# Performance work log

Hardware: AMD Instinct MI355X
Metric: run time of the kernel (lower is better)

## Reference

```python
import jax, jax.numpy as jnp
import numpy as np

B, S, TK, H, E, V, OOV = 16, 8, 400, 256, 128, 50000, 50
H2 = 2 * H


def setup_inputs() -> dict:
    key = jax.random.key(0)
    ks = jax.random.split(key, 24)
    std = 0.02
    d = {}
    d["y_t_1"] = jax.random.randint(ks[0], (B,), 0, V)
    d["h0"] = jax.random.normal(ks[1], (B, H), jnp.float32)
    d["c0"] = jax.random.normal(ks[2], (B, H), jnp.float32)
    d["encoder_output"] = jax.random.normal(ks[3], (B, S, TK, H2), jnp.float32)
    d["section_output"] = jax.random.normal(ks[4], (B, S, H2), jnp.float32)
    d["enc_padding_mask"] = jnp.ones((B, S, TK), jnp.float32)
    d["c_t_1"] = jax.random.normal(ks[5], (B, H2), jnp.float32)
    d["extra_zeros"] = jnp.zeros((B, OOV), jnp.float32)
    d["enc_batch_extend_vocab"] = jax.random.randint(ks[6], (B, S * TK), 0, V + OOV)
    d["coverage"] = jnp.zeros((B, S, TK), jnp.float32)
    d["gamma"] = jnp.ones((B, S, TK), jnp.float32)
    # learned parameters
    d["embedding"] = std * jax.random.normal(ks[7], (V, E), jnp.float32)
    d["W_xc"] = std * jax.random.normal(ks[8], (H2 + E, E), jnp.float32)
    d["b_xc"] = jnp.zeros((E,), jnp.float32)
    d["W_ih"] = std * jax.random.normal(ks[9], (E, 4 * H), jnp.float32)
    d["b_ih"] = jnp.zeros((4 * H,), jnp.float32)
    d["W_hh"] = std * jax.random.normal(ks[10], (H, 4 * H), jnp.float32)
    # pytorch init sets forget-gate bias (2nd quarter) to 1
    d["b_hh"] = jnp.zeros((4 * H,), jnp.float32).at[H:2 * H].set(1.0)
    d["Wh_sec"] = std * jax.random.normal(ks[11], (H2, H2), jnp.float32)
    d["Wd_sec"] = std * jax.random.normal(ks[12], (H2, H2), jnp.float32)
    d["bd_sec"] = jnp.zeros((H2,), jnp.float32)
    d["v_sec"] = std * jax.random.normal(ks[13], (H2, 1), jnp.float32)
    d["Wh_w"] = std * jax.random.normal(ks[14], (H2, H2), jnp.float32)
    d["Wc_w"] = std * jax.random.normal(ks[15], (H2,), jnp.float32)
    d["Wd_w"] = std * jax.random.normal(ks[16], (H2, H2), jnp.float32)
    d["bd_w"] = jnp.zeros((H2,), jnp.float32)
    d["v_w"] = std * jax.random.normal(ks[17], (H2, 1), jnp.float32)
    d["W_pgen"] = std * jax.random.normal(ks[18], (4 * H + E, 1), jnp.float32)
    d["b_pgen"] = jnp.zeros((1,), jnp.float32)
    d["W_out1"] = std * jax.random.normal(ks[19], (3 * H, H), jnp.float32)
    d["b_out1"] = jnp.zeros((H,), jnp.float32)
    d["W_out2"] = std * jax.random.normal(ks[20], (H, V), jnp.float32)
    d["b_out2"] = jnp.zeros((V,), jnp.float32)
    return d


def reference(y_t_1, h0, c0, encoder_output, section_output, enc_padding_mask,
              c_t_1, extra_zeros, enc_batch_extend_vocab, coverage, gamma,
              embedding, W_xc, b_xc, W_ih, b_ih, W_hh, b_hh,
              Wh_sec, Wd_sec, bd_sec, v_sec,
              Wh_w, Wc_w, Wd_w, bd_w, v_w,
              W_pgen, b_pgen, W_out1, b_out1, W_out2, b_out2):
    # embedding + input context projection
    emb = embedding[y_t_1]                                      # [B,E]
    x = jnp.concatenate([c_t_1, emb], axis=1) @ W_xc + b_xc     # [B,E]
    # single-step LSTM (pytorch gate order i,f,g,o)
    gates = x @ W_ih + b_ih + h0 @ W_hh + b_hh                  # [B,4H]
    i, f, g, o = jnp.split(gates, 4, axis=1)
    c = jax.nn.sigmoid(f) * c0 + jax.nn.sigmoid(i) * jnp.tanh(g)
    h = jax.nn.sigmoid(o) * jnp.tanh(c)
    s_t_hat = jnp.concatenate([h, c], axis=1)                   # [B,2H]
    # section attention -> beta [B,S]
    e_sec = jnp.tanh(section_output @ Wh_sec + (s_t_hat @ Wd_sec + bd_sec)[:, None, :])
    sc_sec = jnp.squeeze(e_sec @ v_sec, -1)                     # [B,S]
    beta = jax.nn.softmax(sc_sec, axis=1)
    beta = beta / beta.sum(axis=1, keepdims=True)
    # word attention with coverage feature
    att = encoder_output @ Wh_w + (s_t_hat @ Wd_w + bd_w)[:, None, None, :]
    att = att + coverage[..., None] * Wc_w                      # [B,S,TK,2H]
    sc_w = jnp.squeeze(jnp.tanh(att) @ v_w, -1)                 # [B,S,TK]
    ws = (beta[:, :, None] * sc_w).reshape(B, S * TK)
    mask = enc_padding_mask.reshape(B, S * TK)
    ad = jax.nn.softmax(ws, axis=1) * mask
    attn = ad / ad.sum(axis=1, keepdims=True)                   # [B,S*TK]
    c_t = jnp.einsum('bt,btn->bn', attn, encoder_output.reshape(B, S * TK, H2))
    cov = coverage + attn.reshape(B, S, TK)
    # pointer-gen gate
    p_gen = jax.nn.sigmoid(jnp.concatenate([c_t, s_t_hat, x], axis=1) @ W_pgen + b_pgen)  # [B,1]
    # output vocab distribution
    out = jnp.concatenate([h, c_t], axis=1) @ W_out1 + b_out1
    vocab_dist = jax.nn.softmax(out @ W_out2 + b_out2, axis=1)  # [B,V]
    vd = jnp.concatenate([p_gen * vocab_dist, extra_zeros], axis=1)  # [B,V+OOV]
    ad_ = (1.0 - p_gen) * attn
    rows = jnp.arange(B)[:, None]
    final_dist = vd.at[rows, enc_batch_extend_vocab].add(ad_)
    return (final_dist, h, c, c_t, attn, p_gen, cov)
```

## Files before the change

kernel.cpp:

```cpp
#include <hip/hip_runtime.h>
#include <math.h>

#define BB   16
#define SS   8
#define TKK  400
#define HH   256
#define EE   128
#define VV   50000
#define OOVV 50
#define HH2  512
#define STK  (SS*TKK)
#define VOO  (VV+OOVV)

#define OFF_X     0
#define OFF_ST    2048
#define OFF_SD    10240
#define OFF_WD    18432
#define OFF_SCSEC 26752
#define OFF_SCW   26880
#define OFF_CT    78080
#define OFF_OUT1  86272
#define OFF_PGEN  90368
#define OFF_PSUM  93520
#define OFF_BT    113040

#define O_FD   0
#define O_H    800800
#define O_C    804896
#define O_CT   808992
#define O_ATTN 817184
#define O_PGEN 868384
#define O_COV  868400

#define NLB 391
#define GEMM_NB 800

typedef __attribute__((ext_vector_type(8))) short bf16x8;
typedef __attribute__((ext_vector_type(4))) float f32x4;

__device__ __forceinline__ float sigm(float x){ return 1.0f/(1.0f+expf(-x)); }

__device__ __forceinline__ unsigned short f2b(float f){
  unsigned int u = __float_as_uint(f);
  unsigned int r = (u + 0x7fffu + ((u >> 16) & 1u)) >> 16;
  return (unsigned short)r;
}

__device__ __forceinline__ float tanhfast(float x){
  float cx = fminf(9.0f, fmaxf(-9.0f, x));
  float t = __expf(2.0f*cx);
  return (t - 1.0f) * __builtin_amdgcn_rcpf(t + 1.0f);
}

__device__ __forceinline__ float wave_sum(float v){
  #pragma unroll
  for(int o=32;o>0;o>>=1) v += __shfl_xor(v,o);
  return v;
}
__device__ __forceinline__ float wave_max(float v){
  #pragma unroll
  for(int o=32;o>0;o>>=1) v = fmaxf(v,__shfl_xor(v,o));
  return v;
}

__device__ __forceinline__ void glds16(const void* g, void* l){
  __builtin_amdgcn_global_load_lds((const __attribute__((address_space(1))) void*)g,
                                   (__attribute__((address_space(3))) void*)l, 16, 0, 0);
}

__device__ __forceinline__ bf16x8 cvt8(float4 a, float4 b){
  union{ bf16x8 v; unsigned short u[8]; } t;
  t.u[0]=f2b(a.x); t.u[1]=f2b(a.y); t.u[2]=f2b(a.z); t.u[3]=f2b(a.w);
  t.u[4]=f2b(b.x); t.u[5]=f2b(b.y); t.u[6]=f2b(b.z); t.u[7]=f2b(b.w);
  return t.v;
}

__global__ void k_pre(const float* __restrict__ Whw, unsigned short* __restrict__ Btg,
                      const int* __restrict__ y, const float* __restrict__ ct1,
                      const float* __restrict__ emb, const float* __restrict__ Wxc,
                      const float* __restrict__ bxc, const float* __restrict__ bdsec,
                      const float* __restrict__ bdw, float* __restrict__ ws){
  __shared__ float sm[10440];
  int bi = blockIdx.x, tid = threadIdx.x;
  if(bi < 64){
    int n0 = (bi & 7)*64, k0 = (bi >> 3)*64;
    int tx = tid & 63, ty = tid >> 6;
    #pragma unroll
    for(int it=0; it<16; it++){
      int kk = it*4 + ty;
      sm[kk*65 + tx] = Whw[(size_t)(k0+kk)*HH2 + n0 + tx];
    }
    __syncthreads();
    #pragma unroll
    for(int it=0; it<2; it++){
      int kgl = it*4 + ty;
      int kgG = (k0 >> 3) + kgl;
      int rnd = kgG >> 2, kg = kgG & 3;
      int col = n0 + tx;
      union{ bf16x8 v; unsigned short u[8]; } t;
      #pragma unroll
      for(int j=0;j<8;j++) t.u[j] = f2b(sm[(kgl*8+j)*65 + tx]);
      *(bf16x8*)&Btg[(size_t)rnd*16384 + (size_t)(col*4 + (kg ^ ((col>>1)&3)))*8] = t.v;
    }
  } else if(bi < 80){
    float* cat = sm;
    float* red = sm + 10240;
    for(int f=tid; f<BB*640; f+=256){
      int b = f/640, r = f - b*640;
      cat[f] = (r < HH2) ? ct1[b*HH2 + r] : emb[(size_t)y[b]*EE + (r-HH2)];
    }
    __syncthreads();
    int c = (bi-64)*8 + (tid & 7);
    int b = (tid >> 3) & 15;
    int kh = tid >> 7;
    float acc = 0.0f;
    const float* a = &cat[b*640];
    for(int k=kh*320; k<kh*320+320; k++) acc += a[k]*Wxc[k*EE + c];
    if(kh==1) red[b*8 + (tid&7)] = acc;
    __syncthreads();
    if(kh==0) ws[OFF_X + b*EE + c] = acc + red[b*8 + (tid&7)] + bxc[c];
  } else {
    for(int f=tid; f<BB*HH2; f+=256){
      int c = f & (HH2-1);
      ws[OFF_CT + f] = 0.0f;
      ws[OFF_SD + f] = bdsec[c];
      ws[OFF_WD + f] = bdw[c];
    }
  }
}

__global__ void k_lstm(const float* __restrict__ h0, const float* __restrict__ c0,
                       const float* __restrict__ Wih, const float* __restrict__ bih,
                       const float* __restrict__ Whh, const float* __restrict__ bhh,
                       float* __restrict__ ws, float* __restrict__ out){
  __shared__ float xh[4*384];
  __shared__ float red[3*64*4];
  int tid = threadIdx.x;
  int jc = (blockIdx.x & 15)*16, bc = (blockIdx.x >> 4)*4;
  for(int f=tid; f<4*384; f+=256){
    int bl = f/384, r = f - bl*384;
    xh[f] = (r < EE) ? ws[OFF_X + (bc+bl)*EE + r] : h0[(bc+bl)*HH + (r-EE)];
  }
  __syncthreads();
  int jl = tid & 15, bl = (tid >> 4) & 3, kq = tid >> 6;
  int j = jc + jl, b = bc + bl;
  float a0=0.f, a1=0.f, a2=0.f, a3=0.f;
  const float* a = &xh[bl*384];
  for(int k=kq*96; k<kq*96+96; k++){
    float v = a[k];
    const float* w = (k < EE) ? &Wih[k*4*HH + j] : &Whh[(k-EE)*4*HH + j];
    a0 += v*w[0]; a1 += v*w[HH]; a2 += v*w[2*HH]; a3 += v*w[3*HH];
  }
  if(kq){
    float* r = &red[((kq-1)*64 + bl*16 + jl)*4];
    r[0]=a0; r[1]=a1; r[2]=a2; r[3]=a3;
  }
  __syncthreads();
  if(kq==0){
    #pragma unroll
    for(int p=0;p<3;p++){
      const float* r = &red[(p*64 + bl*16 + jl)*4];
      a0+=r[0]; a1+=r[1]; a2+=r[2]; a3+=r[3];
    }
    a0 += bih[j] + bhh[j];
    a1 += bih[j+HH] + bhh[j+HH];
    a2 += bih[j+2*HH] + bhh[j+2*HH];
    a3 += bih[j+3*HH] + bhh[j+3*HH];
    float c = sigm(a1)*c0[b*HH+j] + sigm(a0)*tanhf(a2);
    float h = sigm(a3)*tanhf(c);
    out[O_H + b*HH + j] = h;
    out[O_C + b*HH + j] = c;
    ws[OFF_ST + b*HH2 + j]      = h;
    ws[OFF_ST + b*HH2 + HH + j] = c;
  }
}

__global__ void k_proj(const float* __restrict__ Wdsec, const float* __restrict__ Wdw,
                       float* __restrict__ ws){
  __shared__ float st[BB*32];
  int tid = threadIdx.x;
  int mi = blockIdx.x >> 5;
  int cb = (blockIdx.x >> 4) & 1;
  int kq = blockIdx.x & 15;
  int k0 = kq*32;
  for(int f=tid; f<BB*32; f+=256){
    int b = f >> 5, kk = f & 31;
    st[f] = ws[OFF_ST + b*HH2 + k0 + kk];
  }
  __syncthreads();
  int c = cb*256 + tid;
  const float* Wm = (mi ? Wdw : Wdsec) + (size_t)k0*HH2 + c;
  float acc[BB];
  #pragma unroll
  for(int b=0;b<BB;b++) acc[b] = 0.0f;
  #pragma unroll 4
  for(int kk=0;kk<32;kk++){
    float wv = Wm[(size_t)kk*HH2];
    #pragma unroll
    for(int b=0;b<BB;b++) acc[b] += st[b*32 + kk]*wv;
  }
  int dst = mi ? OFF_WD : OFF_SD;
  #pragma unroll
  for(int b=0;b<BB;b++) atomicAdd(&ws[dst + b*HH2 + c], acc[b]);
}

__global__ __launch_bounds__(512, 4) void k_gemm6(
        const float* __restrict__ A, const unsigned short* __restrict__ Btg,
        const float* __restrict__ Wcw, const float* __restrict__ vw,
        const float* __restrict__ cover,
        const float* __restrict__ sec, const float* __restrict__ Whsec,
        const float* __restrict__ vsec, float* __restrict__ ws){
  __shared__ __align__(16) unsigned short smem[32768];
  int tid = threadIdx.x;
  if(blockIdx.x >= GEMM_NB){
    float* row = (float*)smem;
    float* red = row + HH2;
    int bi = blockIdx.x - GEMM_NB;
    int b = bi >> 3;
    if(tid < HH2) row[tid] = sec[(size_t)bi*HH2 + tid];
    __syncthreads();
    int col = tid;
    float acc = 0.0f;
    #pragma unroll 8
    for(int k=0;k<HH2;k++) acc += row[k]*Whsec[k*HH2 + col];
    float val = tanhf(acc + ws[OFF_SD + b*HH2 + col]) * vsec[col];
    val = wave_sum(val);
    if((tid&63)==0) red[tid>>6] = val;
    __syncthreads();
    if(tid==0){
      float s = 0.0f;
      #pragma unroll
      for(int i=0;i<8;i++) s += red[i];
      ws[OFF_SCSEC + bi] = s;
    }
    return;
  }
  int w = tid >> 6, lane = tid & 63, m = lane & 15, q = lane >> 4;
  int mk = (m >> 1) & 3, sw = q ^ mk;
  int rg = w >> 2, cg = w & 3;
  int row0 = blockIdx.x * 64;
  int b = blockIdx.x / 50;

  const float* a0p = &A[(size_t)(row0 + rg*32 + m)*HH2 + q*8];
  const float* a1p = a0p + (size_t)16*HH2;

  f32x4 acc0[8], acc1[8];
  #pragma unroll
  for(int j=0;j<8;j++){ acc0[j] = (f32x4){0.f,0.f,0.f,0.f}; acc1[j] = (f32x4){0.f,0.f,0.f,0.f}; }

  float4 pa[2][4];
  bf16x8 af0, af1;

  #define GLDSB(rr, buf) {                                                     \
    const unsigned short* bsrc_ = Btg + (size_t)(rr)*16384;                    \
    unsigned short* ldst_ = &smem[(buf)*16384];                                \
    _Pragma("unroll")                                                          \
    for(int i_=0;i_<4;i_++)                                                    \
      glds16(bsrc_ + i_*4096 + tid*8, ldst_ + i_*4096 + tid*8);                \
  }
  #define LOADA(rr, s) {                                                       \
    pa[s][0] = *(const float4*)(a0p + (rr)*32);                                \
    pa[s][1] = *(const float4*)(a0p + (rr)*32 + 4);                            \
    pa[s][2] = *(const float4*)(a1p + (rr)*32);                                \
    pa[s][3] = *(const float4*)(a1p + (rr)*32 + 4);                            \
  }

  GLDSB(0, 0);
  LOADA(0, 0);
  LOADA(1, 1);
  GLDSB(1, 1);
  asm volatile("s_waitcnt vmcnt(8)" ::: "memory");
  __builtin_amdgcn_sched_barrier(0);
  af0 = cvt8(pa[0][0], pa[0][1]);
  af1 = cvt8(pa[0][2], pa[0][3]);
  __builtin_amdgcn_s_barrier();

  #pragma unroll
  for(int r=0; r<16; r++){
    if(r <= 13) LOADA(r+2, r&1);
    __builtin_amdgcn_s_setprio(1);
    #pragma unroll
    for(int cf=0; cf<8; cf++){
      int col = cg*128 + cf*16 + m;
      bf16x8 bv = *(const bf16x8*)&smem[(r&1)*16384 + ((size_t)col*4 + sw)*8];
      acc0[cf] = __builtin_amdgcn_mfma_f32_16x16x32_bf16(af0, bv, acc0[cf], 0,0,0);
      acc1[cf] = __builtin_amdgcn_mfma_f32_16x16x32_bf16(af1, bv, acc1[cf], 0,0,0);
    }
    __builtin_amdgcn_s_setprio(0);
    if(r <= 13){
      asm volatile("s_waitcnt lgkmcnt(0)" ::: "memory");
      __builtin_amdgcn_sched_barrier(0);
      __builtin_amdgcn_s_barrier();
      GLDSB(r+2, r&1);
    }
    if(r <= 14){
      if(r <= 13){ asm volatile("s_waitcnt vmcnt(8)" ::: "memory"); }
      else       { asm volatile("s_waitcnt vmcnt(0)" ::: "memory"); }
      __builtin_amdgcn_sched_barrier(0);
      af0 = cvt8(pa[(r+1)&1][0], pa[(r+1)&1][1]);
      af1 = cvt8(pa[(r+1)&1][2], pa[(r+1)&1][3]);
      __builtin_amdgcn_s_barrier();
    }
  }
  #undef GLDSB
  #undef LOADA

  float cov0[4], cov1[4];
  #pragma unroll
  for(int r=0;r<4;r++){
    cov0[r] = cover[row0 + rg*32 + q*4 + r];
    cov1[r] = cover[row0 + rg*32 + 16 + q*4 + r];
  }
  float rs0[4] = {0,0,0,0}, rs1[4] = {0,0,0,0};
  #pragma unroll
  for(int j=0;j<8;j++){
    int col = cg*128 + j*16 + m;
    float wdv = ws[OFF_WD + b*HH2 + col];
    float wcv = Wcw[col], vwv = vw[col];
    #pragma unroll
    for(int r=0;r<4;r++){
      rs0[r] += tanhfast(acc0[j][r] + wdv + cov0[r]*wcv) * vwv;
      rs1[r] += tanhfast(acc1[j][r] + wdv + cov1[r]*wcv) * vwv;
    }
  }
  __syncthreads();
  float* rbuf = (float*)smem;
  #pragma unroll
  for(int r=0;r<4;r++){
    float v = rs0[r];
    v += __shfl_xor(v,1,16); v += __shfl_xor(v,2,16);
    v += __shfl_xor(v,4,16); v += __shfl_xor(v,8,16);
    if(m==0) rbuf[cg*64 + rg*32 + q*4 + r] = v;
    float u = rs1[r];
    u += __shfl_xor(u,1,16); u += __shfl_xor(u,2,16);
    u += __shfl_xor(u,4,16); u += __shfl_xor(u,8,16);
    if(m==0) rbuf[cg*64 + rg*32 + 16 + q*4 + r] = u;
  }
  __syncthreads();
  if(tid < 64)
    ws[OFF_SCW + row0 + tid] = rbuf[tid] + rbuf[64+tid] + rbuf[128+tid] + rbuf[192+tid];
}

__global__ void k_attn(const float* __restrict__ mask, const float* __restrict__ cover,
                       float* __restrict__ ws, float* __restrict__ out){
  int b = blockIdx.x, tid = threadIdx.x;
  __shared__ float vals[STK];
  __shared__ float redm[16], reds[16];
  __shared__ float sc[SS];
  if(tid < SS) sc[tid] = ws[OFF_SCSEC + b*SS + tid];
  __syncthreads();
  float bm = -1e30f;
  #pragma unroll
  for(int s=0;s<SS;s++) bm = fmaxf(bm, sc[s]);
  float be[SS]; float bsum = 0.0f;
  #pragma unroll
  for(int s=0;s<SS;s++){ be[s] = expf(sc[s]-bm); bsum += be[s]; }
  #pragma unroll
  for(int s=0;s<SS;s++) be[s] /= bsum;
  int lane = tid & 63, w = tid >> 6;
  float m = -1e30f;
  for(int j=tid;j<STK;j+=1024){
    float v = be[j/TKK] * ws[OFF_SCW + b*STK + j];
    vals[j] = v; m = fmaxf(m, v);
  }
  m = wave_max(m);
  if(lane==0) redm[w] = m;
  __syncthreads();
  if(tid < 16){
    float t = redm[tid];
    #pragma unroll
    for(int o=8;o>0;o>>=1) t = fmaxf(t, __shfl_xor(t,o,16));
    if(tid==0) redm[0] = t;
  }
  __syncthreads();
  m = redm[0];
  float ssum = 0.0f;
  for(int j=tid;j<STK;j+=1024){
    float e = expf(vals[j]-m) * mask[b*STK + j];
    vals[j] = e; ssum += e;
  }
  ssum = wave_sum(ssum);
  if(lane==0) reds[w] = ssum;
  __syncthreads();
  if(tid < 16){
    float t = reds[tid];
    #pragma unroll
    for(int o=8;o>0;o>>=1) t += __shfl_xor(t,o,16);
    if(tid==0) reds[0] = t;
  }
  __syncthreads();
  float inv = 1.0f/reds[0];
  for(int j=tid;j<STK;j+=1024){
    float a = vals[j]*inv;
    out[O_ATTN + b*STK + j] = a;
    out[O_COV  + b*STK + j] = cover[b*STK + j] + a;
  }
}

__global__ void k_ct(const float* __restrict__ enc, const float* __restrict__ out,
                     float* __restrict__ ws){
  int b = blockIdx.y, tid = threadIdx.x;
  __shared__ float a[64];
  __shared__ float part[512];
  int t0 = blockIdx.x*64;
  if(tid<64) a[tid] = out[O_ATTN + b*STK + t0 + tid];
  __syncthreads();
  int c4 = tid & 127, rh = tid >> 7;
  const float4* e4 = (const float4*)enc;
  size_t base = ((size_t)(b*STK + t0 + rh*32))*128 + c4;
  float4 acc = {0.f,0.f,0.f,0.f};
  #pragma unroll 8
  for(int rr=0; rr<32; rr++){
    float4 v = e4[base + (size_t)rr*128];
    float av = a[rh*32 + rr];
    acc.x += av*v.x; acc.y += av*v.y; acc.z += av*v.z; acc.w += av*v.w;
  }
  if(rh) *(float4*)&part[c4*4] = acc;
  __syncthreads();
  if(!rh){
    float4 o = *(const float4*)&part[c4*4];
    atomicAdd(&ws[OFF_CT + b*HH2 + c4*4 + 0], acc.x + o.x);
    atomicAdd(&ws[OFF_CT + b*HH2 + c4*4 + 1], acc.y + o.y);
    atomicAdd(&ws[OFF_CT + b*HH2 + c4*4 + 2], acc.z + o.z);
    atomicAdd(&ws[OFF_CT + b*HH2 + c4*4 + 3], acc.w + o.w);
  }
}

__global__ void k_out1(const float* __restrict__ Wp, const float* __restrict__ bp,
                       const float* __restrict__ Wo1, const float* __restrict__ bo1,
                       float* __restrict__ ws, float* __restrict__ out){
  __shared__ float cat[BB*768];
  __shared__ float red[3*64];
  int tid = threadIdx.x;
  if(blockIdx.x == 64){
    int w = tid >> 6, lane = tid & 63;
    #pragma unroll
    for(int i=0;i<4;i++){
      int b = w*4 + i;
      float p = 0.0f;
      for(int k=lane;k<4*HH+EE;k+=64){
        float val = (k < HH2) ? ws[OFF_CT + b*HH2 + k]
                  : (k < 4*HH) ? ws[OFF_ST + b*HH2 + (k-HH2)]
                  : ws[OFF_X + b*EE + (k-4*HH)];
        p += val * Wp[k];
      }
      p = wave_sum(p);
      if(lane==0){
        float pg = sigm(p + bp[0]);
        ws[OFF_PGEN + b] = pg;
        out[O_PGEN + b]  = pg;
      }
    }
    for(int f=tid; f<BB*HH2; f+=256) out[O_CT + f] = ws[OFF_CT + f];
    return;
  }
  for(int f=tid; f<BB*768; f+=256){
    int b = f/768, r = f - b*768;
    cat[f] = (r < HH) ? ws[OFF_ST + b*HH2 + r] : ws[OFF_CT + b*HH2 + (r-HH)];
  }
  __syncthreads();
  int cl = tid & 3, bl = (tid >> 2) & 15, kq = tid >> 6;
  int c = blockIdx.x*4 + cl;
  float acc = 0.0f;
  const float* a = &cat[bl*768];
  for(int k=kq*192; k<kq*192+192; k++) acc += a[k]*Wo1[k*HH + c];
  if(kq) red[(kq-1)*64 + bl*4 + cl] = acc;
  __syncthreads();
  if(kq==0){
    acc += red[bl*4+cl] + red[64 + bl*4+cl] + red[128 + bl*4+cl];
    ws[OFF_OUT1 + bl*HH + c] = acc + bo1[c];
  }
}

__global__ void k_logits(const float* __restrict__ W2, const float* __restrict__ b2,
                         float* __restrict__ ws, float* __restrict__ out){
  int tid = threadIdx.x;
  __shared__ float o1[BB*HH];
  for(int i=tid;i<BB*HH/4;i+=256)
    ((float4*)o1)[i] = ((const float4*)&ws[OFF_OUT1])[i];
  __syncthreads();
  int cl = tid & 31, bq = tid >> 5;
  int c4 = blockIdx.x*128 + cl*4;
  bool ok = c4 < VV;
  int b0 = bq*2, b1 = b0+1;
  float4 acc0 = {0.f,0.f,0.f,0.f}, acc1 = {0.f,0.f,0.f,0.f};
  if(ok){
    const float* oa = &o1[b0*HH];
    const float* ob = &o1[b1*HH];
    #pragma unroll 4
    for(int k=0;k<HH;k++){
      float4 wv = *(const float4*)&W2[(size_t)k*VV + c4];
      float xa = oa[k], xb = ob[k];
      acc0.x += xa*wv.x; acc0.y += xa*wv.y; acc0.z += xa*wv.z; acc0.w += xa*wv.w;
      acc1.x += xb*wv.x; acc1.y += xb*wv.y; acc1.z += xb*wv.z; acc1.w += xb*wv.w;
    }
  }
  float bv[4] = {0,0,0,0};
  if(ok){ float4 t = *(const float4*)&b2[c4]; bv[0]=t.x; bv[1]=t.y; bv[2]=t.z; bv[3]=t.w; }
  float a0[4] = {acc0.x, acc0.y, acc0.z, acc0.w};
  float a1[4] = {acc1.x, acc1.y, acc1.z, acc1.w};
  float s0 = 0.0f, s1 = 0.0f;
  #pragma unroll
  for(int j=0;j<4;j++){
    float e0 = ok ? expf(a0[j]+bv[j]) : 0.0f;
    float e1 = ok ? expf(a1[j]+bv[j]) : 0.0f;
    if(ok){
      out[(size_t)b0*VOO + c4 + j] = e0;
      out[(size_t)b1*VOO + c4 + j] = e1;
    }
    s0 += e0; s1 += e1;
  }
  #pragma unroll
  for(int o=1;o<32;o<<=1){ s0 += __shfl_xor(s0,o,32); s1 += __shfl_xor(s1,o,32); }
  if(cl==0){
    ws[OFF_PSUM + b0*NLB + blockIdx.x] = s0;
    ws[OFF_PSUM + b1*NLB + blockIdx.x] = s1;
  }
}

__global__ void k_final(const float* __restrict__ xz, float* __restrict__ ws,
                        float* __restrict__ out){
  int b = blockIdx.y;
  int v = blockIdx.x*256 + threadIdx.x;
  __shared__ float red[4];
  int lane = threadIdx.x & 63, w = threadIdx.x >> 6;
  float p = 0.0f;
  for(int i=threadIdx.x;i<NLB;i+=256) p += ws[OFF_PSUM + b*NLB + i];
  p = wave_sum(p);
  if(lane==0) red[w] = p;
  __syncthreads();
  float s = red[0]+red[1]+red[2]+red[3];
  float pg = ws[OFF_PGEN + b];
  if(v < VV)       out[(size_t)b*VOO + v] = pg * out[(size_t)b*VOO + v] / s;
  else if(v < VOO) out[(size_t)b*VOO + v] = xz[b*OOVV + (v-VV)];
}

__global__ void k_scatter(const int* __restrict__ ebev, float* __restrict__ ws,
                          float* __restrict__ out){
  int b = blockIdx.y;
  float r = 1.0f - ws[OFF_PGEN + b];
  for(int j=blockIdx.x*256+threadIdx.x;j<STK;j+=1024){
    int idx = ebev[b*STK + j];
    atomicAdd(&out[(size_t)b*VOO + idx], r*out[O_ATTN + b*STK + j]);
  }
}

extern "C" void kernel_launch(void* const* d_in, const int* in_sizes, int n_in,
                              void* d_out, int out_size, void* d_ws, size_t ws_size,
                              hipStream_t stream){
  const int*   y     = (const int*)  d_in[0];
  const float* h0    = (const float*)d_in[1];
  const float* c0    = (const float*)d_in[2];
  const float* enc   = (const float*)d_in[3];
  const float* sec   = (const float*)d_in[4];
  const float* mask  = (const float*)d_in[5];
  const float* ct1   = (const float*)d_in[6];
  const float* xz    = (const float*)d_in[7];
  const int*   ebev  = (const int*)  d_in[8];
  const float* cover = (const float*)d_in[9];
  const float* emb   = (const float*)d_in[11];
  const float* Wxc   = (const float*)d_in[12];
  const float* bxc   = (const float*)d_in[13];
  const float* Wih   = (const float*)d_in[14];
  const float* bih   = (const float*)d_in[15];
  const float* Whh   = (const float*)d_in[16];
  const float* bhh   = (const float*)d_in[17];
  const float* Whsec = (const float*)d_in[18];
  const float* Wdsec = (const float*)d_in[19];
  const float* bdsec = (const float*)d_in[20];
  const float* vsec  = (const float*)d_in[21];
  const float* Whw   = (const float*)d_in[22];
  const float* Wcw   = (const float*)d_in[23];
  const float* Wdw   = (const float*)d_in[24];
  const float* bdw   = (const float*)d_in[25];
  const float* vw    = (const float*)d_in[26];
  const float* Wp    = (const float*)d_in[27];
  const float* bp    = (const float*)d_in[28];
  const float* Wo1   = (const float*)d_in[29];
  const float* bo1   = (const float*)d_in[30];
  const float* Wo2   = (const float*)d_in[31];
  const float* bo2   = (const float*)d_in[32];
  float* out = (float*)d_out;
  float* ws  = (float*)d_ws;
  unsigned short* Btg = (unsigned short*)(ws + OFF_BT);

  k_pre    <<<dim3(81),       dim3(256),  0, stream>>>(Whw, Btg, y, ct1, emb, Wxc, bxc, bdsec, bdw, ws);
  k_lstm   <<<dim3(64),       dim3(256),  0, stream>>>(h0, c0, Wih, bih, Whh, bhh, ws, out);
  k_proj   <<<dim3(64),       dim3(256),  0, stream>>>(Wdsec, Wdw, ws);
  k_gemm6  <<<dim3(928),      dim3(512),  0, stream>>>(enc, Btg, Wcw, vw, cover, sec, Whsec, vsec, ws);
  k_attn   <<<dim3(BB),       dim3(1024), 0, stream>>>(mask, cover, ws, out);
  k_ct     <<<dim3(50,BB),    dim3(256),  0, stream>>>(enc, out, ws);
  k_out1   <<<dim3(65),       dim3(256),  0, stream>>>(Wp, bp, Wo1, bo1, ws, out);
  k_logits <<<dim3(NLB),      dim3(256),  0, stream>>>(Wo2, bo2, ws, out);
  k_final  <<<dim3(196,BB),   dim3(256),  0, stream>>>(xz, ws, out);
  k_scatter<<<dim3(4,BB),     dim3(256),  0, stream>>>(ebev, ws, out);
}
```

Measured before the change: 530.3 us.

## Single-buffer A-operand prefetch and drop main loop unroll in attention GEMM

Replaces the two-stage register prefetch of the fp32 encoder tile with a single-stage prefetch one iteration ahead, adjusting the vmcnt wait accordingly. It also removes full unrolling of the 16-iteration k loop. The aim is to lower register pressure and code size, possibly raising occupancy, at the cost of less latency hiding for global loads.

```diff
diff --git a/kernel.cpp b/kernel.cpp
--- a/kernel.cpp
+++ b/kernel.cpp
@@ -248,41 +248,39 @@
   #pragma unroll
   for(int j=0;j<8;j++){ acc0[j] = (f32x4){0.f,0.f,0.f,0.f}; acc1[j] = (f32x4){0.f,0.f,0.f,0.f}; }
 
-  float4 pa[2][4];
+  float4 pa0, pa1, pa2, pa3;
   bf16x8 af0, af1;
 
   #define GLDSB(rr, buf) {                                                     \
     const unsigned short* bsrc_ = Btg + (size_t)(rr)*16384;                    \
-    unsigned short* ldst_ = &smem[(buf)*16384];                                \
+    unsigned short* ldst_ = &smem[(size_t)(buf)*16384];                        \
     _Pragma("unroll")                                                          \
     for(int i_=0;i_<4;i_++)                                                    \
       glds16(bsrc_ + i_*4096 + tid*8, ldst_ + i_*4096 + tid*8);                \
   }
-  #define LOADA(rr, s) {                                                       \
-    pa[s][0] = *(const float4*)(a0p + (rr)*32);                                \
-    pa[s][1] = *(const float4*)(a0p + (rr)*32 + 4);                            \
-    pa[s][2] = *(const float4*)(a1p + (rr)*32);                                \
-    pa[s][3] = *(const float4*)(a1p + (rr)*32 + 4);                            \
+  #define LOADA(rr) {                                                          \
+    pa0 = *(const float4*)(a0p + (rr)*32);                                     \
+    pa1 = *(const float4*)(a0p + (rr)*32 + 4);                                 \
+    pa2 = *(const float4*)(a1p + (rr)*32);                                     \
+    pa3 = *(const float4*)(a1p + (rr)*32 + 4);                                 \
   }
 
   GLDSB(0, 0);
-  LOADA(0, 0);
-  LOADA(1, 1);
+  LOADA(0);
   GLDSB(1, 1);
   asm volatile("s_waitcnt vmcnt(8)" ::: "memory");
   __builtin_amdgcn_sched_barrier(0);
-  af0 = cvt8(pa[0][0], pa[0][1]);
-  af1 = cvt8(pa[0][2], pa[0][3]);
+  af0 = cvt8(pa0, pa1);
+  af1 = cvt8(pa2, pa3);
   __builtin_amdgcn_s_barrier();
 
-  #pragma unroll
   for(int r=0; r<16; r++){
-    if(r <= 13) LOADA(r+2, r&1);
+    if(r < 15) LOADA(r+1);
     __builtin_amdgcn_s_setprio(1);
     #pragma unroll
     for(int cf=0; cf<8; cf++){
       int col = cg*128 + cf*16 + m;
-      bf16x8 bv = *(const bf16x8*)&smem[(r&1)*16384 + ((size_t)col*4 + sw)*8];
+      bf16x8 bv = *(const bf16x8*)&smem[(size_t)(r&1)*16384 + ((size_t)col*4 + sw)*8];
       acc0[cf] = __builtin_amdgcn_mfma_f32_16x16x32_bf16(af0, bv, acc0[cf], 0,0,0);
       acc1[cf] = __builtin_amdgcn_mfma_f32_16x16x32_bf16(af1, bv, acc1[cf], 0,0,0);
     }
@@ -293,12 +291,12 @@
       __builtin_amdgcn_s_barrier();
       GLDSB(r+2, r&1);
     }
-    if(r <= 14){
-      if(r <= 13){ asm volatile("s_waitcnt vmcnt(8)" ::: "memory"); }
+    if(r < 15){
+      if(r <= 13){ asm volatile("s_waitcnt vmcnt(4)" ::: "memory"); }
       else       { asm volatile("s_waitcnt vmcnt(0)" ::: "memory"); }
       __builtin_amdgcn_sched_barrier(0);
-      af0 = cvt8(pa[(r+1)&1][0], pa[(r+1)&1][1]);
-      af1 = cvt8(pa[(r+1)&1][2], pa[(r+1)&1][3]);
+      af0 = cvt8(pa0, pa1);
+      af1 = cvt8(pa2, pa3);
       __builtin_amdgcn_s_barrier();
     }
   }
```

Result: faster. 475.2 us (-10.4%).
